# Kernel tuning notes

Hardware: AMD Instinct MI355X
Metric: run time of the kernel (lower is better)

## Reference

```python
import jax, jax.numpy as jnp
from jax import lax
import numpy as np


def _bn(x, g, b, eps=1e-5):
    # BatchNorm2d in training mode: biased batch stats over (N,H,W) per channel
    m = jnp.mean(x, axis=(0, 2, 3), keepdims=True)
    v = jnp.mean((x - m) ** 2, axis=(0, 2, 3), keepdims=True)
    return (x - m) * lax.rsqrt(v + eps) * g[None, :, None, None] + b[None, :, None, None]


def _conv(x, w, b, pad):
    y = lax.conv_general_dilated(x, w, (1, 1), [(pad, pad), (pad, pad)],
                                 dimension_numbers=('NCHW', 'OIHW', 'NCHW'))
    return y + b[None, :, None, None]


def _prelu(x, a):
    return jnp.where(x >= 0, x, a * x)


def _maxpool2(x):
    return lax.reduce_window(x, -jnp.inf, lax.max, (1, 1, 2, 2), (1, 1, 2, 2), 'VALID')


def _up2(x):
    # UpsamplingBilinear2d(scale_factor=2) -> bilinear, align_corners=True
    B, C, H, W = x.shape
    def idx(n):
        pos = jnp.arange(2 * n, dtype=x.dtype) * (n - 1) / (2 * n - 1)
        lo = jnp.floor(pos).astype(jnp.int32)
        hi = jnp.minimum(lo + 1, n - 1)
        return lo, hi, pos - lo.astype(x.dtype)
    lo, hi, f = idx(H)
    x = x[:, :, lo, :] * (1 - f)[:, None] + x[:, :, hi, :] * f[:, None]
    lo, hi, f = idx(W)
    x = x[:, :, :, lo] * (1 - f) + x[:, :, :, hi] * f
    return x


def _forward(x, n16, sigma16, bias16, prelu_a,
             bn3_g, bn3_b, bn32_g, bn32_b, bn64_g, bn64_b, bn128_g, bn128_b,
             w1, b1, w2, b2, w3, b3, w4, b4, w5, b5, w6, b6, w7, b7, w11, b11):
    B, C, H, W = x.shape
    # 16 enhancement curves fused: r_k = x^{n_k} / (x^{n_k} + sigma_k^{n_k} + bias_k)
    xn = x[None] ** n16[:, None, None, None, None]          # (16,B,3,H,W)
    r = xn / (xn + (sigma16 ** n16)[:, None, None, None, None]
              + bias16[:, None, None, None, None])
    # each branch gets its own BatchNorm2d(3) stats (same affine params)
    r = jax.vmap(lambda t: _bn(t, bn3_g, bn3_b))(r)
    x_fusion = jnp.transpose(r, (1, 0, 2, 3, 4)).reshape(B, 16 * C, H, W)
    x1 = _bn(_maxpool2(_prelu(_conv(x_fusion, w1, b1, 1), prelu_a)), bn32_g, bn32_b)
    x2 = _bn(_maxpool2(_prelu(_conv(x1, w2, b2, 1), prelu_a)), bn64_g, bn64_b)
    x3 = _bn(_maxpool2(_prelu(_conv(x2, w3, b3, 1), prelu_a)), bn128_g, bn128_b)
    x4 = _bn(_conv(x3, w4, b4, 1), bn128_g, bn128_b)
    x5 = _bn(_up2(_prelu(_conv(jnp.concatenate([x4, x3], 1), w5, b5, 1), prelu_a)), bn64_g, bn64_b)
    x6 = _bn(_up2(_prelu(_conv(jnp.concatenate([x2, x5], 1), w6, b6, 1), prelu_a)), bn32_g, bn32_b)
    x_out = jax.nn.sigmoid(_up2(_prelu(_conv(jnp.concatenate([x1, x6], 1), w7, b7, 1), prelu_a)))
    x_out = _conv(x_out, w11, b11, 0)
    x_mean = jnp.mean(x, axis=1, keepdims=True)
    x_out1 = jnp.mean(x_out, axis=1, keepdims=True)
    return x_out1 * (x / (x_mean + 1e-6))


def setup_inputs() -> dict:
    key = jax.random.key(0)
    ks = jax.random.split(key, 16)
    B, H, W = 8, 256, 256
    nf = 32
    x = jax.random.uniform(ks[0], (B, 3, H, W), jnp.float32, 1e-3, 1.0)
    n16 = jnp.arange(1, 17, dtype=jnp.float32) * 0.5
    sigma16 = jnp.full((16,), 0.5, jnp.float32)
    bias16 = jnp.full((16,), 1e-4, jnp.float32)
    prelu_a = jnp.float32(0.25)
    def cw(k, o, i, kk):
        return jax.random.normal(k, (o, i, kk, kk), jnp.float32) * 0.05
    def cb(o):
        return jnp.zeros((o,), jnp.float32)
    return dict(
        x=x, n16=n16, sigma16=sigma16, bias16=bias16, prelu_a=prelu_a,
        bn3_g=jnp.ones((3,), jnp.float32), bn3_b=jnp.zeros((3,), jnp.float32),
        bn32_g=jnp.ones((32,), jnp.float32), bn32_b=jnp.zeros((32,), jnp.float32),
        bn64_g=jnp.ones((64,), jnp.float32), bn64_b=jnp.zeros((64,), jnp.float32),
        bn128_g=jnp.ones((128,), jnp.float32), bn128_b=jnp.zeros((128,), jnp.float32),
        w1=cw(ks[1], nf, 48, 3), b1=cb(nf),
        w2=cw(ks[2], 2 * nf, nf, 3), b2=cb(2 * nf),
        w3=cw(ks[3], 4 * nf, 2 * nf, 3), b3=cb(4 * nf),
        w4=cw(ks[4], 4 * nf, 4 * nf, 3), b4=cb(4 * nf),
        w5=cw(ks[5], 2 * nf, 8 * nf, 3), b5=cb(2 * nf),
        w6=cw(ks[6], nf, 4 * nf, 3), b6=cb(nf),
        w7=cw(ks[7], nf, 2 * nf, 3), b7=cb(nf),
        w11=cw(ks[8], 3, nf, 1), b11=cb(3),
    )


def reference(x, n16, sigma16, bias16, prelu_a,
              bn3_g, bn3_b, bn32_g, bn32_b, bn64_g, bn64_b, bn128_g, bn128_b,
              w1, b1, w2, b2, w3, b3, w4, b4, w5, b5, w6, b6, w7, b7, w11, b11):
    return _forward(x, n16, sigma16, bias16, prelu_a,
                    bn3_g, bn3_b, bn32_g, bn32_b, bn64_g, bn64_b, bn128_g, bn128_b,
                    w1, b1, w2, b2, w3, b3, w4, b4, w5, b5, w6, b6, w7, b7, w11, b11)
```

## Files before the change

### kernel.cpp

```cpp
#include <hip/hip_runtime.h>

#define FAST_EXP2(x) __builtin_amdgcn_exp2f(x)
#define FAST_LOG2(x) __builtin_amdgcn_logf(x)
#define FAST_RCP(x)  __builtin_amdgcn_rcpf(x)

static constexpr size_t S3_SUM=0,   S3_SQ=48;
static constexpr size_t S32A_SUM=96,  S32A_SQ=128;
static constexpr size_t S64A_SUM=160, S64A_SQ=224;
static constexpr size_t S128A_SUM=288,S128A_SQ=416;
static constexpr size_t S128B_SUM=544,S128B_SQ=672;
static constexpr size_t S64B_SUM=800, S64B_SQ=864;
static constexpr size_t S32B_SUM=928, S32B_SQ=960;
static constexpr size_t A3_=1024,  B3_=1072;
static constexpr size_t A32A_=1120, B32A_=1152;
static constexpr size_t A64A_=1184, B64A_=1248;
static constexpr size_t A128A_=1312,B128A_=1440;
static constexpr size_t A128B_=1568,B128B_=1696;
static constexpr size_t A64B_=1824, B64B_=1888;
static constexpr size_t A32B_=1952, B32B_=1984;
static constexpr size_t SPB_=2016, WBAR_=2032, BBAR_=2064;
static constexpr size_t XF_=4096;
static constexpr size_t T1_=XF_+25165824;
static constexpr size_t T2_=T1_+4194304;
static constexpr size_t T3_=T2_+2097152;
static constexpr size_t T4_=T3_+1048576;
static constexpr size_t C5_=T4_+1048576;
static constexpr size_t U5_=C5_+524288;
static constexpr size_t C6_=U5_+2097152;
static constexpr size_t U6_=C6_+1048576;
static constexpr size_t C7_=U6_+4194304;

__global__ void k_precomp(const float* __restrict__ n16, const float* __restrict__ sig16,
                          const float* __restrict__ b16, const float* __restrict__ w11,
                          const float* __restrict__ b11,
                          float* __restrict__ spb, float* __restrict__ wbar, float* __restrict__ bbar)
{
    int t = threadIdx.x;
    if (t < 16) spb[t] = powf(sig16[t], n16[t]) + b16[t];
    else if (t < 48) { int j = t - 16; wbar[j] = (w11[j] + w11[32 + j] + w11[64 + j]) * (1.f/3.f); }
    else if (t == 48) bbar[0] = (b11[0] + b11[1] + b11[2]) * (1.f/3.f);
}

__global__ __launch_bounds__(256) void k_branch_stats(
    const float* __restrict__ x, const float* __restrict__ n16,
    const float* __restrict__ sig16, const float* __restrict__ b16,
    float* __restrict__ sum, float* __restrict__ sq)
{
    const int c = blockIdx.x >> 6;
    const int chunk = blockIdx.x & 63;
    float nk[16], den[16];
#pragma unroll
    for (int k = 0; k < 16; ++k) { nk[k] = n16[k]; den[k] = powf(sig16[k], nk[k]) + b16[k]; }
    float s[16], q[16];
#pragma unroll
    for (int k = 0; k < 16; ++k) { s[k] = 0.f; q[k] = 0.f; }
    const int per = 8192;
    int start = chunk * per;
    for (int i = start + (int)threadIdx.x; i < start + per; i += 256) {
        int b = i >> 16, hw = i & 65535;
        float xv = x[(size_t)(b*3 + c)*65536 + hw];
        float t = FAST_LOG2(xv);
#pragma unroll
        for (int k = 0; k < 16; ++k) {
            float v = FAST_EXP2(nk[k]*t);
            float r = v * FAST_RCP(v + den[k]);
            s[k] += r; q[k] += r*r;
        }
    }
    __shared__ float red[4][32];
    int lane = threadIdx.x & 63, wid = threadIdx.x >> 6;
#pragma unroll
    for (int k = 0; k < 16; ++k) {
#pragma unroll
        for (int off = 32; off > 0; off >>= 1) {
            s[k] += __shfl_down(s[k], off);
            q[k] += __shfl_down(q[k], off);
        }
    }
    if (lane == 0) {
#pragma unroll
        for (int k = 0; k < 16; ++k) { red[wid][k] = s[k]; red[wid][16+k] = q[k]; }
    }
    __syncthreads();
    if (threadIdx.x < 32) {
        float v = red[0][threadIdx.x] + red[1][threadIdx.x] + red[2][threadIdx.x] + red[3][threadIdx.x];
        int k = threadIdx.x & 15;
        if (threadIdx.x < 16) atomicAdd(&sum[k*3 + c], v);
        else                  atomicAdd(&sq[k*3 + c], v);
    }
}

__global__ __launch_bounds__(256) void k_stats(
    const float* __restrict__ in, int C, int HW, int nchunks, int per,
    float* __restrict__ sum, float* __restrict__ sq)
{
    int c = blockIdx.x / nchunks;
    int chunk = blockIdx.x - c*nchunks;
    float s = 0.f, q = 0.f;
    int start = chunk * per, end = start + per;
    for (int i = start + (int)threadIdx.x; i < end; i += 256) {
        int b = i / HW, hw = i - b*HW;
        float v = in[((size_t)b*C + c)*HW + hw];
        s += v; q += v*v;
    }
#pragma unroll
    for (int off = 32; off > 0; off >>= 1) { s += __shfl_down(s, off); q += __shfl_down(q, off); }
    __shared__ float ss[4], qq[4];
    int lane = threadIdx.x & 63, wid = threadIdx.x >> 6;
    if (lane == 0) { ss[wid] = s; qq[wid] = q; }
    __syncthreads();
    if (threadIdx.x == 0) {
        atomicAdd(&sum[c], ss[0]+ss[1]+ss[2]+ss[3]);
        atomicAdd(&sq[c],  qq[0]+qq[1]+qq[2]+qq[3]);
    }
}

__global__ void k_finalize(const float* __restrict__ sum, const float* __restrict__ sq,
                           const float* __restrict__ g, const float* __restrict__ bb,
                           int C, int gdim, float invN,
                           float* __restrict__ A, float* __restrict__ Bs)
{
    int i = blockIdx.x*blockDim.x + threadIdx.x;
    if (i < C) {
        float m   = sum[i]*invN;
        float var = fmaxf(sq[i]*invN - m*m, 0.f);
        float inv = rsqrtf(var + 1e-5f);
        float a   = g[i % gdim]*inv;
        A[i]  = a;
        Bs[i] = bb[i % gdim] - m*a;
    }
}

__global__ __launch_bounds__(256) void k_fusion(
    const float* __restrict__ x, const float* __restrict__ n16, const float* __restrict__ spb,
    const float* __restrict__ A, const float* __restrict__ Bs, float* __restrict__ out)
{
    int idx = blockIdx.x*256 + threadIdx.x;
    if (idx >= 8*3*65536) return;
    int hw = idx & 65535;
    int bc = idx >> 16;
    int b = bc / 3, c = bc - b*3;
    float xv = x[idx];
    float t = FAST_LOG2(xv);
    size_t obase = ((size_t)b*48 + c)*65536 + hw;
#pragma unroll
    for (int k = 0; k < 16; ++k) {
        float v = FAST_EXP2(n16[k]*t);
        float r = v * FAST_RCP(v + spb[k]);
        int ch = k*3 + c;
        out[obase + (size_t)(k*3)*65536] = r*A[ch] + Bs[ch];
    }
}

__global__ __launch_bounds__(256) void k_fill(
    float* __restrict__ out, const float* __restrict__ bias, int C, int HW, int total)
{
    int idx = blockIdx.x*256 + threadIdx.x;
    if (idx < total) {
        int c = (idx / HW) % C;
        out[idx] = bias[c];
    }
}

template<int COG, bool POOL>
__global__ __launch_bounds__(256,4) void k_conv_big(
    const float* __restrict__ in1, int C1,
    const float* __restrict__ sc1, const float* __restrict__ sh1,
    const float* __restrict__ in2, int C2,
    const float* __restrict__ sc2, const float* __restrict__ sh2,
    const float* __restrict__ w, const float* __restrict__ bias,
    int Cout, int H, int W, const float* __restrict__ prelu_a, int do_prelu,
    float* __restrict__ out)
{
    const int Cin = C1 + C2;
    const int tx = threadIdx.x & 15, ty = threadIdx.x >> 4;
    const int nco = Cout / COG;
    const int b = blockIdx.z / nco, cob = (blockIdx.z - b*nco)*COG;
    const int x0 = blockIdx.x*64, y0 = blockIdx.y*32;

    __shared__ float wl[COG*64*9];
    __shared__ float tile[2][34*68];

    for (int t = threadIdx.x; t < COG*Cin*9; t += 256) {
        int co = t % COG; int rest = t / COG;
        int k = rest % 9; int ci = rest / 9;
        wl[t] = w[(((size_t)(cob+co))*Cin + ci)*9 + k];
    }

    float acc[COG][8];
#pragma unroll
    for (int i = 0; i < COG; ++i)
#pragma unroll
        for (int j = 0; j < 8; ++j) acc[i][j] = 0.f;

#pragma unroll 1
    for (int cb = 0; cb < Cin; cb += 2) {
#pragma unroll
        for (int sub = 0; sub < 2; ++sub) {
            int ci = cb + sub;
            const float* in; int cc; const float* scp; const float* shp; int Cn;
            if (ci < C1) { in = in1; cc = ci;      scp = sc1; shp = sh1; Cn = C1; }
            else         { in = in2; cc = ci - C1; scp = sc2; shp = sh2; Cn = C2; }
            float scv = scp ? scp[cc] : 1.f;
            float shv = scp ? shp[cc] : 0.f;
            const float* base = in + ((size_t)b*Cn + cc)*H*W;
#pragma unroll 1
            for (int i = threadIdx.x; i < 34*66; i += 256) {
                int r = i / 66, c = i - r*66;
                int gy = y0 - 1 + r, gx = x0 - 1 + c;
                float v = 0.f;
                if ((unsigned)gy < (unsigned)H && (unsigned)gx < (unsigned)W)
                    v = base[(size_t)gy*W + gx]*scv + shv;
                tile[sub][r*68 + c] = v;
            }
        }
        __syncthreads();
#pragma unroll
        for (int sub = 0; sub < 2; ++sub) {
            const float* tl = &tile[sub][(2*ty)*68 + 4*tx];
            float iv[4][6];
#pragma unroll
            for (int r = 0; r < 4; ++r) {
                float4 av = *(const float4*)(tl + r*68);
                float2 bv = *(const float2*)(tl + r*68 + 4);
                iv[r][0]=av.x; iv[r][1]=av.y; iv[r][2]=av.z; iv[r][3]=av.w;
                iv[r][4]=bv.x; iv[r][5]=bv.y;
            }
            const float* wbase = &wl[(cb+sub)*9*COG];
#pragma unroll
            for (int kh = 0; kh < 3; ++kh)
#pragma unroll
            for (int kw = 0; kw < 3; ++kw) {
                const int k = kh*3 + kw;
                float wv[COG];
#pragma unroll
                for (int q = 0; q < COG/4; ++q) {
                    float4 wq = *((const float4*)(wbase + k*COG) + q);
                    wv[4*q+0]=wq.x; wv[4*q+1]=wq.y; wv[4*q+2]=wq.z; wv[4*q+3]=wq.w;
                }
#pragma unroll
                for (int co = 0; co < COG; ++co)
#pragma unroll
                    for (int py = 0; py < 2; ++py)
#pragma unroll
                        for (int px = 0; px < 4; ++px)
                            acc[co][py*4+px] += wv[co]*iv[py+kh][px+kw];
            }
        }
        __syncthreads();
    }

    float a = __ldg(prelu_a);
    if (POOL) {
        const int Hp = H >> 1, Wp = W >> 1;
        int pyp = (y0 >> 1) + ty, pxp = (x0 >> 1) + 2*tx;
#pragma unroll
        for (int co = 0; co < COG; ++co) {
            float bv = bias[cob + co];
            float v[8];
#pragma unroll
            for (int p = 0; p < 8; ++p) {
                float t = acc[co][p] + bv;
                v[p] = t >= 0.f ? t : a*t;
            }
            float2 st;
            st.x = fmaxf(fmaxf(v[0], v[1]), fmaxf(v[4], v[5]));
            st.y = fmaxf(fmaxf(v[2], v[3]), fmaxf(v[6], v[7]));
            *(float2*)(out + (((size_t)b*Cout + cob + co)*Hp + pyp)*Wp + pxp) = st;
        }
    } else {
        int oy = y0 + 2*ty, ox = x0 + 4*tx;
#pragma unroll
        for (int co = 0; co < COG; ++co) {
            float bv = bias[cob + co];
            float* op = out + (((size_t)b*Cout + cob + co)*H + oy)*W + ox;
#pragma unroll
            for (int py = 0; py < 2; ++py) {
                float4 st;
                float t0 = acc[co][py*4+0] + bv, t1 = acc[co][py*4+1] + bv;
                float t2 = acc[co][py*4+2] + bv, t3 = acc[co][py*4+3] + bv;
                if (do_prelu) {
                    t0 = t0 >= 0.f ? t0 : a*t0; t1 = t1 >= 0.f ? t1 : a*t1;
                    t2 = t2 >= 0.f ? t2 : a*t2; t3 = t3 >= 0.f ? t3 : a*t3;
                }
                st.x=t0; st.y=t1; st.z=t2; st.w=t3;
                *(float4*)(op + py*W) = st;
            }
        }
    }
}

template<int COG>
__global__ __launch_bounds__(256,4) void k_conv_sm(
    const float* __restrict__ in1, int C1,
    const float* __restrict__ sc1, const float* __restrict__ sh1,
    const float* __restrict__ in2, int C2,
    const float* __restrict__ sc2, const float* __restrict__ sh2,
    const float* __restrict__ w,
    int Cout, int H, int W, int ciN, int nsplit,
    float* __restrict__ out)
{
    const int Cin = C1 + C2;
    const int tx = threadIdx.x & 15, ty = threadIdx.x >> 4;
    const int nco = Cout / COG;
    int z = blockIdx.z;
    const int sp = z % nsplit; z /= nsplit;
    const int b = z / nco, cob = (z - b*nco)*COG;
    const int ci0 = sp * ciN;
    const int x0 = blockIdx.x*32, y0 = blockIdx.y*32;

    __shared__ float wl[COG*32*9];
    __shared__ float tile[2][34*36];

    for (int t = threadIdx.x; t < COG*ciN*9; t += 256) {
        int co = t % COG; int rest = t / COG;
        int k = rest % 9; int ci = rest / 9;
        wl[t] = w[(((size_t)(cob+co))*Cin + ci0 + ci)*9 + k];
    }

    float acc[COG][4];
#pragma unroll
    for (int i = 0; i < COG; ++i)
#pragma unroll
        for (int j = 0; j < 4; ++j) acc[i][j] = 0.f;

#pragma unroll 1
    for (int cb = 0; cb < ciN; cb += 2) {
#pragma unroll
        for (int sub = 0; sub < 2; ++sub) {
            int ci = ci0 + cb + sub;
            const float* in; int cc; const float* scp; const float* shp; int Cn;
            if (ci < C1) { in = in1; cc = ci;      scp = sc1; shp = sh1; Cn = C1; }
            else         { in = in2; cc = ci - C1; scp = sc2; shp = sh2; Cn = C2; }
            float scv = scp ? scp[cc] : 1.f;
            float shv = scp ? shp[cc] : 0.f;
            const float* base = in + ((size_t)b*Cn + cc)*H*W;
#pragma unroll 1
            for (int i = threadIdx.x; i < 34*34; i += 256) {
                int r = i / 34, c = i - r*34;
                int gy = y0 - 1 + r, gx = x0 - 1 + c;
                float v = 0.f;
                if ((unsigned)gy < (unsigned)H && (unsigned)gx < (unsigned)W)
                    v = base[(size_t)gy*W + gx]*scv + shv;
                tile[sub][r*36 + c] = v;
            }
        }
        __syncthreads();
#pragma unroll
        for (int sub = 0; sub < 2; ++sub) {
            const float* tl = &tile[sub][(2*ty)*36 + 2*tx];
            float iv[4][4];
#pragma unroll
            for (int r = 0; r < 4; ++r) {
                float2 a2 = *(const float2*)(tl + r*36);
                float2 b2 = *(const float2*)(tl + r*36 + 2);
                iv[r][0]=a2.x; iv[r][1]=a2.y; iv[r][2]=b2.x; iv[r][3]=b2.y;
            }
            const float* wbase = &wl[(cb+sub)*9*COG];
#pragma unroll
            for (int kh = 0; kh < 3; ++kh)
#pragma unroll
            for (int kw = 0; kw < 3; ++kw) {
                const int k = kh*3 + kw;
                float wv[COG];
#pragma unroll
                for (int q = 0; q < COG/4; ++q) {
                    float4 wq = *((const float4*)(wbase + k*COG) + q);
                    wv[4*q+0]=wq.x; wv[4*q+1]=wq.y; wv[4*q+2]=wq.z; wv[4*q+3]=wq.w;
                }
#pragma unroll
                for (int co = 0; co < COG; ++co)
#pragma unroll
                    for (int py = 0; py < 2; ++py)
#pragma unroll
                        for (int px = 0; px < 2; ++px)
                            acc[co][py*2+px] += wv[co]*iv[py+kh][px+kw];
            }
        }
        __syncthreads();
    }

    int oy = y0 + 2*ty, ox = x0 + 2*tx;
#pragma unroll
    for (int co = 0; co < COG; ++co) {
        float* op = out + (((size_t)b*Cout + cob + co)*H + oy)*W + ox;
        atomicAdd(&op[0],     acc[co][0]);
        atomicAdd(&op[1],     acc[co][1]);
        atomicAdd(&op[W],     acc[co][2]);
        atomicAdd(&op[W + 1], acc[co][3]);
    }
}

__global__ __launch_bounds__(256) void k_up2(
    const float* __restrict__ in, float* __restrict__ out, int BC, int h, int w,
    const float* __restrict__ prelu_a, int do_prelu)
{
    int idx = blockIdx.x*256 + threadIdx.x;
    int W2 = 2*w, H2 = 2*h;
    int total = BC*H2*W2;
    if (idx >= total) return;
    float a = do_prelu ? __ldg(prelu_a) : 0.f;
    int ox = idx % W2; int t = idx / W2; int oy = t % H2; int bc = t / H2;
    float py = ((float)oy * (float)(h-1)) / (float)(2*h - 1);
    int ly = (int)floorf(py); int hy = min(ly+1, h-1); float fy = py - (float)ly;
    float px = ((float)ox * (float)(w-1)) / (float)(2*w - 1);
    int lx = (int)floorf(px); int hx = min(lx+1, w-1); float fx = px - (float)lx;
    const float* p = in + (size_t)bc*h*w;
    float v00 = p[(size_t)ly*w + lx], v01 = p[(size_t)ly*w + hx];
    float v10 = p[(size_t)hy*w + lx], v11 = p[(size_t)hy*w + hx];
    if (do_prelu) {
        v00 = v00 >= 0.f ? v00 : a*v00;
        v01 = v01 >= 0.f ? v01 : a*v01;
        v10 = v10 >= 0.f ? v10 : a*v10;
        v11 = v11 >= 0.f ? v11 : a*v11;
    }
    float v0 = v00*(1.f-fx) + v01*fx;
    float v1 = v10*(1.f-fx) + v11*fx;
    out[idx] = v0*(1.f-fy) + v1*fy;
}

__global__ __launch_bounds__(256) void k_final(
    const float* __restrict__ c7, const float* __restrict__ x,
    const float* __restrict__ wbar, const float* __restrict__ bbar,
    float* __restrict__ out)
{
    int idx = blockIdx.x*256 + threadIdx.x;
    if (idx >= 8*65536) return;
    int hw = idx & 65535, b = idx >> 16;
    int oy = hw >> 8, ox = hw & 255;
    float py = ((float)oy * 127.f) / 255.f;
    int ly = (int)floorf(py); int hy = min(ly+1, 127); float fy = py - (float)ly;
    float px = ((float)ox * 127.f) / 255.f;
    int lx = (int)floorf(px); int hx = min(lx+1, 127); float fx = px - (float)lx;
    float w00 = (1.f-fy)*(1.f-fx), w01 = (1.f-fy)*fx, w10 = fy*(1.f-fx), w11v = fy*fx;
    const float* base = c7 + (size_t)b*32*16384;
    float accum = bbar[0];
#pragma unroll 8
    for (int j = 0; j < 32; ++j) {
        const float* p = base + (size_t)j*16384;
        float v = p[ly*128 + lx]*w00 + p[ly*128 + hx]*w01 + p[hy*128 + lx]*w10 + p[hy*128 + hx]*w11v;
        float s = FAST_RCP(1.f + __expf(-v));
        accum += wbar[j]*s;
    }
    size_t xb = (size_t)b*3*65536 + hw;
    float x0 = x[xb], x1 = x[xb + 65536], x2 = x[xb + 2*65536];
    float m = (x0 + x1 + x2)*(1.f/3.f) + 1e-6f;
    float sc = accum * FAST_RCP(m);
    out[xb]            = sc*x0;
    out[xb + 65536]    = sc*x1;
    out[xb + 2*65536]  = sc*x2;
}

extern "C" void kernel_launch(void* const* d_in, const int* in_sizes, int n_in,
                              void* d_out, int out_size, void* d_ws, size_t ws_size,
                              hipStream_t stream) {
    const float* x       = (const float*)d_in[0];
    const float* n16     = (const float*)d_in[1];
    const float* sig16   = (const float*)d_in[2];
    const float* bia16   = (const float*)d_in[3];
    const float* prelu_a = (const float*)d_in[4];
    const float* bn3_g   = (const float*)d_in[5];
    const float* bn3_b   = (const float*)d_in[6];
    const float* bn32_g  = (const float*)d_in[7];
    const float* bn32_b  = (const float*)d_in[8];
    const float* bn64_g  = (const float*)d_in[9];
    const float* bn64_b  = (const float*)d_in[10];
    const float* bn128_g = (const float*)d_in[11];
    const float* bn128_b = (const float*)d_in[12];
    const float* w1 = (const float*)d_in[13]; const float* b1 = (const float*)d_in[14];
    const float* w2 = (const float*)d_in[15]; const float* b2 = (const float*)d_in[16];
    const float* w3 = (const float*)d_in[17]; const float* b3 = (const float*)d_in[18];
    const float* w4 = (const float*)d_in[19]; const float* b4 = (const float*)d_in[20];
    const float* w5 = (const float*)d_in[21]; const float* b5 = (const float*)d_in[22];
    const float* w6 = (const float*)d_in[23]; const float* b6 = (const float*)d_in[24];
    const float* w7 = (const float*)d_in[25]; const float* b7 = (const float*)d_in[26];
    const float* w11= (const float*)d_in[27]; const float* b11= (const float*)d_in[28];
    float* ws  = (float*)d_ws;
    float* out = (float*)d_out;

    (void)hipMemsetAsync(d_ws, 0, 4096*sizeof(float), stream);

    k_precomp<<<1, 64, 0, stream>>>(n16, sig16, bia16, w11, b11, ws+SPB_, ws+WBAR_, ws+BBAR_);

    k_branch_stats<<<192, 256, 0, stream>>>(x, n16, sig16, bia16, ws+S3_SUM, ws+S3_SQ);
    k_finalize<<<1, 128, 0, stream>>>(ws+S3_SUM, ws+S3_SQ, bn3_g, bn3_b, 48, 3, 1.f/524288.f, ws+A3_, ws+B3_);
    k_fusion<<<6144, 256, 0, stream>>>(x, n16, ws+SPB_, ws+A3_, ws+B3_, ws+XF_);

    k_conv_big<8,true><<<dim3(4,8,32), 256, 0, stream>>>(
        ws+XF_, 48, nullptr, nullptr, nullptr, 0, nullptr, nullptr,
        w1, b1, 32, 256, 256, prelu_a, 1, ws+T1_);
    k_stats<<<2048, 256, 0, stream>>>(ws+T1_, 32, 16384, 64, 2048, ws+S32A_SUM, ws+S32A_SQ);
    k_finalize<<<1, 128, 0, stream>>>(ws+S32A_SUM, ws+S32A_SQ, bn32_g, bn32_b, 32, 32, 1.f/131072.f, ws+A32A_, ws+B32A_);

    k_conv_big<4,true><<<dim3(2,4,128), 256, 0, stream>>>(
        ws+T1_, 32, ws+A32A_, ws+B32A_, nullptr, 0, nullptr, nullptr,
        w2, b2, 64, 128, 128, prelu_a, 1, ws+T2_);
    k_stats<<<1024, 256, 0, stream>>>(ws+T2_, 64, 4096, 16, 2048, ws+S64A_SUM, ws+S64A_SQ);
    k_finalize<<<1, 128, 0, stream>>>(ws+S64A_SUM, ws+S64A_SQ, bn64_g, bn64_b, 64, 64, 1.f/32768.f, ws+A64A_, ws+B64A_);

    k_conv_big<4,true><<<dim3(1,2,256), 256, 0, stream>>>(
        ws+T2_, 64, ws+A64A_, ws+B64A_, nullptr, 0, nullptr, nullptr,
        w3, b3, 128, 64, 64, prelu_a, 1, ws+T3_);
    k_stats<<<512, 256, 0, stream>>>(ws+T3_, 128, 1024, 4, 2048, ws+S128A_SUM, ws+S128A_SQ);
    k_finalize<<<1, 128, 0, stream>>>(ws+S128A_SUM, ws+S128A_SQ, bn128_g, bn128_b, 128, 128, 1.f/8192.f, ws+A128A_, ws+B128A_);

    k_fill<<<4096, 256, 0, stream>>>(ws+T4_, b4, 128, 1024, 1048576);
    k_conv_sm<8><<<dim3(1,1,512), 256, 0, stream>>>(
        ws+T3_, 128, ws+A128A_, ws+B128A_, nullptr, 0, nullptr, nullptr,
        w4, 128, 32, 32, 32, 4, ws+T4_);
    k_stats<<<512, 256, 0, stream>>>(ws+T4_, 128, 1024, 4, 2048, ws+S128B_SUM, ws+S128B_SQ);
    k_finalize<<<1, 128, 0, stream>>>(ws+S128B_SUM, ws+S128B_SQ, bn128_g, bn128_b, 128, 128, 1.f/8192.f, ws+A128B_, ws+B128B_);

    k_fill<<<2048, 256, 0, stream>>>(ws+C5_, b5, 64, 1024, 524288);
    k_conv_sm<8><<<dim3(1,1,512), 256, 0, stream>>>(
        ws+T4_, 128, ws+A128B_, ws+B128B_, ws+T3_, 128, ws+A128A_, ws+B128A_,
        w5, 64, 32, 32, 32, 8, ws+C5_);
    k_up2<<<8192, 256, 0, stream>>>(ws+C5_, ws+U5_, 8*64, 32, 32, prelu_a, 1);
    k_stats<<<1024, 256, 0, stream>>>(ws+U5_, 64, 4096, 16, 2048, ws+S64B_SUM, ws+S64B_SQ);
    k_finalize<<<1, 128, 0, stream>>>(ws+S64B_SUM, ws+S64B_SQ, bn64_g, bn64_b, 64, 64, 1.f/32768.f, ws+A64B_, ws+B64B_);

    k_fill<<<4096, 256, 0, stream>>>(ws+C6_, b6, 32, 4096, 1048576);
    k_conv_sm<8><<<dim3(2,2,128), 256, 0, stream>>>(
        ws+T2_, 64, ws+A64A_, ws+B64A_, ws+U5_, 64, ws+A64B_, ws+B64B_,
        w6, 32, 64, 64, 32, 4, ws+C6_);
    k_up2<<<16384, 256, 0, stream>>>(ws+C6_, ws+U6_, 8*32, 64, 64, prelu_a, 1);
    k_stats<<<2048, 256, 0, stream>>>(ws+U6_, 32, 16384, 64, 2048, ws+S32B_SUM, ws+S32B_SQ);
    k_finalize<<<1, 128, 0, stream>>>(ws+S32B_SUM, ws+S32B_SQ, bn32_g, bn32_b, 32, 32, 1.f/131072.f, ws+A32B_, ws+B32B_);

    k_conv_big<4,false><<<dim3(2,4,64), 256, 0, stream>>>(
        ws+T1_, 32, ws+A32A_, ws+B32A_, ws+U6_, 32, ws+A32B_, ws+B32B_,
        w7, b7, 32, 128, 128, prelu_a, 1, ws+C7_);

    k_final<<<2048, 256, 0, stream>>>(ws+C7_, x, ws+WBAR_, ws+BBAR_, out);
}
```

Before: 1.684 ms.

## Fuse enhancement-curve generation into first conv and retile remaining convolutions

Removes the separate fusion kernel that materialised the 48-channel enhanced tensor. The first conv now recomputes the 16 curve responses per tile in shared memory from log2(x), with the BN3 affine folded in. This drops a large global write and read-back but repeats the exp2/rcp work on the halo pixels. The other convolutions are rebuilt: the small-tile kernel gains bias, PReLU and pool epilogues plus an optional non-split mode, conv3 and conv7 move to 32x32 tiles with 8 output channels, and conv2 uses 8 output channels per block.

```diff
diff --git a/kernel.cpp b/kernel.cpp
--- a/kernel.cpp
+++ b/kernel.cpp
@@ -19,8 +19,7 @@
 static constexpr size_t A64B_=1824, B64B_=1888;
 static constexpr size_t A32B_=1952, B32B_=1984;
 static constexpr size_t SPB_=2016, WBAR_=2032, BBAR_=2064;
-static constexpr size_t XF_=4096;
-static constexpr size_t T1_=XF_+25165824;
+static constexpr size_t T1_=4096;
 static constexpr size_t T2_=T1_+4194304;
 static constexpr size_t T3_=T2_+2097152;
 static constexpr size_t T4_=T3_+1048576;
@@ -131,27 +130,6 @@
     }
 }
 
-__global__ __launch_bounds__(256) void k_fusion(
-    const float* __restrict__ x, const float* __restrict__ n16, const float* __restrict__ spb,
-    const float* __restrict__ A, const float* __restrict__ Bs, float* __restrict__ out)
-{
-    int idx = blockIdx.x*256 + threadIdx.x;
-    if (idx >= 8*3*65536) return;
-    int hw = idx & 65535;
-    int bc = idx >> 16;
-    int b = bc / 3, c = bc - b*3;
-    float xv = x[idx];
-    float t = FAST_LOG2(xv);
-    size_t obase = ((size_t)b*48 + c)*65536 + hw;
-#pragma unroll
-    for (int k = 0; k < 16; ++k) {
-        float v = FAST_EXP2(n16[k]*t);
-        float r = v * FAST_RCP(v + spb[k]);
-        int ch = k*3 + c;
-        out[obase + (size_t)(k*3)*65536] = r*A[ch] + Bs[ch];
-    }
-}
-
 __global__ __launch_bounds__(256) void k_fill(
     float* __restrict__ out, const float* __restrict__ bias, int C, int HW, int total)
 {
@@ -162,17 +140,129 @@
     }
 }
 
+template<int COG>
+__global__ __launch_bounds__(256,3) void k_conv1f(
+    const float* __restrict__ x,
+    const float* __restrict__ n16, const float* __restrict__ spb,
+    const float* __restrict__ A, const float* __restrict__ Bs,
+    const float* __restrict__ w, const float* __restrict__ bias,
+    const float* __restrict__ prelu_a,
+    float* __restrict__ out)
+{
+    const int tx = threadIdx.x & 15, ty = threadIdx.x >> 4;
+    const int nco = 32 / COG;
+    const int b = blockIdx.z / nco, cob = (blockIdx.z - b*nco)*COG;
+    const int x0 = blockIdx.x*32, y0 = blockIdx.y*32;
+
+    __shared__ float wl[COG*48*9];
+    __shared__ float tl[3*1224];
+    __shared__ float rl[3*1224];
+    __shared__ float al[48], bl[48], nl[16], dl[16];
+
+    for (int t = threadIdx.x; t < COG*48*9; t += 256) {
+        int co = t % COG; int rest = t / COG;
+        int kk = rest % 9; int ci = rest / 9;
+        wl[t] = w[(((size_t)(cob+co))*48 + ci)*9 + kk];
+    }
+    if (threadIdx.x < 48) { al[threadIdx.x] = A[threadIdx.x]; bl[threadIdx.x] = Bs[threadIdx.x]; }
+    else if (threadIdx.x < 64)  nl[threadIdx.x-48] = n16[threadIdx.x-48];
+    else if (threadIdx.x < 80)  dl[threadIdx.x-64] = spb[threadIdx.x-64];
+
+    int off_[14]; int chpack = 0; int okf = 0;
+#pragma unroll
+    for (int j = 0; j < 14; ++j) {
+        int i = threadIdx.x + 256*j;
+        if (i < 3468) {
+            int ch = i / 1156, jj = i - ch*1156;
+            int rr = jj / 34, cc = jj - rr*34;
+            int gy = y0 - 1 + rr, gx = x0 - 1 + cc;
+            bool ok = (unsigned)gy < 256u && (unsigned)gx < 256u;
+            off_[j] = ch*1224 + rr*36 + cc;
+            chpack |= ch << (2*j);
+            if (ok) {
+                okf |= 1 << j;
+                tl[off_[j]] = FAST_LOG2(x[((size_t)(b*3+ch))*65536 + gy*256 + gx]);
+            } else tl[off_[j]] = 0.f;
+        } else off_[j] = 3671;
+    }
+
+    float acc[COG][4];
+#pragma unroll
+    for (int i = 0; i < COG; ++i)
+#pragma unroll
+        for (int j = 0; j < 4; ++j) acc[i][j] = 0.f;
+
+#pragma unroll 1
+    for (int k = 0; k < 16; ++k) {
+        __syncthreads();
+        float nk = nl[k], dk = dl[k];
+#pragma unroll
+        for (int j = 0; j < 14; ++j) {
+            float rv = 0.f;
+            if (okf & (1 << j)) {
+                int ch = (chpack >> (2*j)) & 3;
+                int chg = k*3 + ch;
+                float v = FAST_EXP2(nk * tl[off_[j]]);
+                rv = v * FAST_RCP(v + dk) * al[chg] + bl[chg];
+            }
+            rl[off_[j]] = rv;
+        }
+        __syncthreads();
+#pragma unroll
+        for (int ch = 0; ch < 3; ++ch) {
+            const float* tlp = &rl[ch*1224 + (2*ty)*36 + 2*tx];
+            float iv[4][4];
+#pragma unroll
+            for (int r = 0; r < 4; ++r) {
+                float2 a2 = *(const float2*)(tlp + r*36);
+                float2 b2 = *(const float2*)(tlp + r*36 + 2);
+                iv[r][0]=a2.x; iv[r][1]=a2.y; iv[r][2]=b2.x; iv[r][3]=b2.y;
+            }
+            const float* wbase = &wl[((k*3+ch)*9)*COG];
+#pragma unroll
+            for (int kh = 0; kh < 3; ++kh)
+#pragma unroll
+            for (int kw = 0; kw < 3; ++kw) {
+                const int kk = kh*3 + kw;
+                float wv[COG];
+#pragma unroll
+                for (int q = 0; q < COG/4; ++q) {
+                    float4 wq = *((const float4*)(wbase + kk*COG) + q);
+                    wv[4*q+0]=wq.x; wv[4*q+1]=wq.y; wv[4*q+2]=wq.z; wv[4*q+3]=wq.w;
+                }
+#pragma unroll
+                for (int co = 0; co < COG; ++co)
+#pragma unroll
+                    for (int py = 0; py < 2; ++py)
+#pragma unroll
+                        for (int px = 0; px < 2; ++px)
+                            acc[co][py*2+px] += wv[co]*iv[py+kh][px+kw];
+            }
+        }
+    }
+
+    float a = __ldg(prelu_a);
+    int pyp = (y0 >> 1) + ty, pxp = (x0 >> 1) + tx;
+#pragma unroll
+    for (int co = 0; co < COG; ++co) {
+        float bv = bias[cob + co];
+        float v0 = acc[co][0] + bv, v1 = acc[co][1] + bv;
+        float v2 = acc[co][2] + bv, v3 = acc[co][3] + bv;
+        v0 = v0 >= 0.f ? v0 : a*v0; v1 = v1 >= 0.f ? v1 : a*v1;
+        v2 = v2 >= 0.f ? v2 : a*v2; v3 = v3 >= 0.f ? v3 : a*v3;
+        out[(((size_t)b*32 + cob + co)*128 + pyp)*128 + pxp] = fmaxf(fmaxf(v0,v1), fmaxf(v2,v3));
+    }
+}
+
 template<int COG, bool POOL>
 __global__ __launch_bounds__(256,4) void k_conv_big(
     const float* __restrict__ in1, int C1,
     const float* __restrict__ sc1, const float* __restrict__ sh1,
-    const float* __restrict__ in2, int C2,
-    const float* __restrict__ sc2, const float* __restrict__ sh2,
     const float* __restrict__ w, const float* __restrict__ bias,
     int Cout, int H, int W, const float* __restrict__ prelu_a, int do_prelu,
     float* __restrict__ out)
 {
-    const int Cin = C1 + C2;
+    const int Cin = C1;
     const int tx = threadIdx.x & 15, ty = threadIdx.x >> 4;
     const int nco = Cout / COG;
     const int b = blockIdx.z / nco, cob = (blockIdx.z - b*nco)*COG;
@@ -198,12 +288,9 @@
 #pragma unroll
         for (int sub = 0; sub < 2; ++sub) {
             int ci = cb + sub;
-            const float* in; int cc; const float* scp; const float* shp; int Cn;
-            if (ci < C1) { in = in1; cc = ci;      scp = sc1; shp = sh1; Cn = C1; }
-            else         { in = in2; cc = ci - C1; scp = sc2; shp = sh2; Cn = C2; }
-            float scv = scp ? scp[cc] : 1.f;
-            float shv = scp ? shp[cc] : 0.f;
-            const float* base = in + ((size_t)b*Cn + cc)*H*W;
+            float scv = sc1 ? sc1[ci] : 1.f;
+            float shv = sc1 ? sh1[ci] : 0.f;
+            const float* base = in1 + ((size_t)b*Cin + ci)*H*W;
 #pragma unroll 1
             for (int i = threadIdx.x; i < 34*66; i += 256) {
                 int r = i / 66, c = i - r*66;
@@ -290,14 +377,15 @@
     }
 }
 
-template<int COG>
-__global__ __launch_bounds__(256,4) void k_conv_sm(
+template<int COG, int MAXCI, bool POOL, bool SPLIT>
+__global__ __launch_bounds__(256,4) void k_conv32(
     const float* __restrict__ in1, int C1,
     const float* __restrict__ sc1, const float* __restrict__ sh1,
     const float* __restrict__ in2, int C2,
     const float* __restrict__ sc2, const float* __restrict__ sh2,
-    const float* __restrict__ w,
-    int Cout, int H, int W, int ciN, int nsplit,
+    const float* __restrict__ w, const float* __restrict__ bias,
+    int Cout, int H, int W, const float* __restrict__ prelu_a, int do_prelu,
+    int ciN, int nsplit,
     float* __restrict__ out)
 {
     const int Cin = C1 + C2;
@@ -309,7 +397,7 @@
     const int ci0 = sp * ciN;
     const int x0 = blockIdx.x*32, y0 = blockIdx.y*32;
 
-    __shared__ float wl[COG*32*9];
+    __shared__ float wl[COG*MAXCI*9];
     __shared__ float tile[2][34*36];
 
     for (int t = threadIdx.x; t < COG*ciN*9; t += 256) {
@@ -380,14 +468,45 @@
         __syncthreads();
     }
 
-    int oy = y0 + 2*ty, ox = x0 + 2*tx;
-#pragma unroll
-    for (int co = 0; co < COG; ++co) {
-        float* op = out + (((size_t)b*Cout + cob + co)*H + oy)*W + ox;
-        atomicAdd(&op[0],     acc[co][0]);
-        atomicAdd(&op[1],     acc[co][1]);
-        atomicAdd(&op[W],     acc[co][2]);
-        atomicAdd(&op[W + 1], acc[co][3]);
+    if (SPLIT) {
+        int oy = y0 + 2*ty, ox = x0 + 2*tx;
+#pragma unroll
+        for (int co = 0; co < COG; ++co) {
+            float* op = out + (((size_t)b*Cout + cob + co)*H + oy)*W + ox;
+            atomicAdd(&op[0],     acc[co][0]);
+            atomicAdd(&op[1],     acc[co][1]);
+            atomicAdd(&op[W],     acc[co][2]);
+            atomicAdd(&op[W + 1], acc[co][3]);
+        }
+    } else {
+        float a = __ldg(prelu_a);
+        if (POOL) {
+            const int Hp = H >> 1, Wp = W >> 1;
+            int pyp = (y0 >> 1) + ty, pxp = (x0 >> 1) + tx;
+#pragma unroll
+            for (int co = 0; co < COG; ++co) {
+                float bv = bias[cob + co];
+                float v0 = acc[co][0] + bv, v1 = acc[co][1] + bv;
+                float v2 = acc[co][2] + bv, v3 = acc[co][3] + bv;
+                v0 = v0 >= 0.f ? v0 : a*v0; v1 = v1 >= 0.f ? v1 : a*v1;
+                v2 = v2 >= 0.f ? v2 : a*v2; v3 = v3 >= 0.f ? v3 : a*v3;
+                out[(((size_t)b*Cout + cob + co)*Hp + pyp)*Wp + pxp] = fmaxf(fmaxf(v0,v1), fmaxf(v2,v3));
+            }
+        } else {
+            int oy = y0 + 2*ty, ox = x0 + 2*tx;
+#pragma unroll
+            for (int co = 0; co < COG; ++co) {
+                float bv = bias[cob + co];
+                float* op = out + (((size_t)b*Cout + cob + co)*H + oy)*W + ox;
+                float v0 = acc[co][0] + bv, v1 = acc[co][1] + bv;
+                float v2 = acc[co][2] + bv, v3 = acc[co][3] + bv;
+                if (do_prelu) {
+                    v0 = v0 >= 0.f ? v0 : a*v0; v1 = v1 >= 0.f ? v1 : a*v1;
+                    v2 = v2 >= 0.f ? v2 : a*v2; v3 = v3 >= 0.f ? v3 : a*v3;
+                }
+                op[0] = v0; op[1] = v1; op[W] = v2; op[W+1] = v3;
+            }
+        }
     }
 }
 
@@ -484,52 +603,49 @@
 
     k_branch_stats<<<192, 256, 0, stream>>>(x, n16, sig16, bia16, ws+S3_SUM, ws+S3_SQ);
     k_finalize<<<1, 128, 0, stream>>>(ws+S3_SUM, ws+S3_SQ, bn3_g, bn3_b, 48, 3, 1.f/524288.f, ws+A3_, ws+B3_);
-    k_fusion<<<6144, 256, 0, stream>>>(x, n16, ws+SPB_, ws+A3_, ws+B3_, ws+XF_);
-
-    k_conv_big<8,true><<<dim3(4,8,32), 256, 0, stream>>>(
-        ws+XF_, 48, nullptr, nullptr, nullptr, 0, nullptr, nullptr,
-        w1, b1, 32, 256, 256, prelu_a, 1, ws+T1_);
+
+    k_conv1f<8><<<dim3(8,8,32), 256, 0, stream>>>(x, n16, ws+SPB_, ws+A3_, ws+B3_,
+                                                  w1, b1, prelu_a, ws+T1_);
     k_stats<<<2048, 256, 0, stream>>>(ws+T1_, 32, 16384, 64, 2048, ws+S32A_SUM, ws+S32A_SQ);
     k_finalize<<<1, 128, 0, stream>>>(ws+S32A_SUM, ws+S32A_SQ, bn32_g, bn32_b, 32, 32, 1.f/131072.f, ws+A32A_, ws+B32A_);
 
-    k_conv_big<4,true><<<dim3(2,4,128), 256, 0, stream>>>(
-        ws+T1_, 32, ws+A32A_, ws+B32A_, nullptr, 0, nullptr, nullptr,
-        w2, b2, 64, 128, 128, prelu_a, 1, ws+T2_);
+    k_conv_big<8,true><<<dim3(2,4,64), 256, 0, stream>>>(
+        ws+T1_, 32, ws+A32A_, ws+B32A_, w2, b2, 64, 128, 128, prelu_a, 1, ws+T2_);
     k_stats<<<1024, 256, 0, stream>>>(ws+T2_, 64, 4096, 16, 2048, ws+S64A_SUM, ws+S64A_SQ);
     k_finalize<<<1, 128, 0, stream>>>(ws+S64A_SUM, ws+S64A_SQ, bn64_g, bn64_b, 64, 64, 1.f/32768.f, ws+A64A_, ws+B64A_);
 
-    k_conv_big<4,true><<<dim3(1,2,256), 256, 0, stream>>>(
+    k_conv32<8,64,true,false><<<dim3(2,2,128), 256, 0, stream>>>(
         ws+T2_, 64, ws+A64A_, ws+B64A_, nullptr, 0, nullptr, nullptr,
-        w3, b3, 128, 64, 64, prelu_a, 1, ws+T3_);
+        w3, b3, 128, 64, 64, prelu_a, 1, 64, 1, ws+T3_);
     k_stats<<<512, 256, 0, stream>>>(ws+T3_, 128, 1024, 4, 2048, ws+S128A_SUM, ws+S128A_SQ);
     k_finalize<<<1, 128, 0, stream>>>(ws+S128A_SUM, ws+S128A_SQ, bn128_g, bn128_b, 128, 128, 1.f/8192.f, ws+A128A_, ws+B128A_);
 
     k_fill<<<4096, 256, 0, stream>>>(ws+T4_, b4, 128, 1024, 1048576);
-    k_conv_sm<8><<<dim3(1,1,512), 256, 0, stream>>>(
+    k_conv32<8,32,false,true><<<dim3(1,1,512), 256, 0, stream>>>(
         ws+T3_, 128, ws+A128A_, ws+B128A_, nullptr, 0, nullptr, nullptr,
-        w4, 128, 32, 32, 32, 4, ws+T4_);
+        w4, nullptr, 128, 32, 32, prelu_a, 0, 32, 4, ws+T4_);
     k_stats<<<512, 256, 0, stream>>>(ws+T4_, 128, 1024, 4, 2048, ws+S128B_SUM, ws+S128B_SQ);
     k_finalize<<<1, 128, 0, stream>>>(ws+S128B_SUM, ws+S128B_SQ, bn128_g, bn128_b, 128, 128, 1.f/8192.f, ws+A128B_, ws+B128B_);
 
     k_fill<<<2048, 256, 0, stream>>>(ws+C5_, b5, 64, 1024, 524288);
-    k_conv_sm<8><<<dim3(1,1,512), 256, 0, stream>>>(
+    k_conv32<8,32,false,true><<<dim3(1,1,512), 256, 0, stream>>>(
         ws+T4_, 128, ws+A128B_, ws+B128B_, ws+T3_, 128, ws+A128A_, ws+B128A_,
-        w5, 64, 32, 32, 32, 8, ws+C5_);
+        w5, nullptr, 64, 32, 32, prelu_a, 0, 32, 8, ws+C5_);
     k_up2<<<8192, 256, 0, stream>>>(ws+C5_, ws+U5_, 8*64, 32, 32, prelu_a, 1);
     k_stats<<<1024, 256, 0, stream>>>(ws+U5_, 64, 4096, 16, 2048, ws+S64B_SUM, ws+S64B_SQ);
     k_finalize<<<1, 128, 0, stream>>>(ws+S64B_SUM, ws+S64B_SQ, bn64_g, bn64_b, 64, 64, 1.f/32768.f, ws+A64B_, ws+B64B_);
 
     k_fill<<<4096, 256, 0, stream>>>(ws+C6_, b6, 32, 4096, 1048576);
-    k_conv_sm<8><<<dim3(2,2,128), 256, 0, stream>>>(
+    k_conv32<8,32,false,true><<<dim3(2,2,128), 256, 0, stream>>>(
         ws+T2_, 64, ws+A64A_, ws+B64A_, ws+U5_, 64, ws+A64B_, ws+B64B_,
-        w6, 32, 64, 64, 32, 4, ws+C6_);
+        w6, nullptr, 32, 64, 64, prelu_a, 0, 32, 4, ws+C6_);
     k_up2<<<16384, 256, 0, stream>>>(ws+C6_, ws+U6_, 8*32, 64, 64, prelu_a, 1);
     k_stats<<<2048, 256, 0, stream>>>(ws+U6_, 32, 16384, 64, 2048, ws+S32B_SUM, ws+S32B_SQ);
     k_finalize<<<1, 128, 0, stream>>>(ws+S32B_SUM, ws+S32B_SQ, bn32_g, bn32_b, 32, 32, 1.f/131072.f, ws+A32B_, ws+B32B_);
 
-    k_conv_big<4,false><<<dim3(2,4,64), 256, 0, stream>>>(
+    k_conv32<8,64,false,false><<<dim3(4,4,32), 256, 0, stream>>>(
         ws+T1_, 32, ws+A32A_, ws+B32A_, ws+U6_, 32, ws+A32B_, ws+B32B_,
-        w7, b7, 32, 128, 128, prelu_a, 1, ws+C7_);
+        w7, b7, 32, 128, 128, prelu_a, 1, 64, 1, ws+C7_);
 
     k_final<<<2048, 256, 0, stream>>>(ws+C7_, x, ws+WBAR_, ws+BBAR_, out);
 }
```

Measured after the change: 1.447 ms. 14.1% less time.
